# Kernel optimization log

Hardware: AMD Instinct MI355X
Metric: run time of the kernel (lower is better)

Reference implementation:

```python
import jax, jax.numpy as jnp
import numpy as np
import math

ROPE_THETA = 10000.0


def apply_rope(x, positions):
    # x: [B, H, S, d_k], positions: [S]
    d_k = x.shape[-1]
    inv_freq = 1.0 / (ROPE_THETA ** (jnp.arange(0, d_k, 2, dtype=jnp.float32) / d_k))  # [d_k/2]
    angles = positions.astype(jnp.float32)[:, None] * inv_freq[None, :]  # [S, d_k/2]
    cos = jnp.cos(angles)
    sin = jnp.sin(angles)
    x1 = x[..., 0::2]
    x2 = x[..., 1::2]
    r1 = x1 * cos - x2 * sin
    r2 = x1 * sin + x2 * cos
    out = jnp.stack([r1, r2], axis=-1)  # interleave pairs back
    return out.reshape(x.shape)


def setup_inputs() -> dict:
    key = jax.random.key(0)
    k1, k2, k3 = jax.random.split(key, 3)
    B, S, D = 4, 2048, 1024
    x = jax.random.normal(k1, (B, S, D), dtype=jnp.float32)
    token_positions = jnp.arange(S, dtype=jnp.int32)
    w_qkv = jax.random.normal(k2, (3 * D, D), dtype=jnp.float32) * (1.0 / math.sqrt(D))
    w_o = jax.random.normal(k3, (D, D), dtype=jnp.float32) * (1.0 / math.sqrt(D))
    return {"x": x, "token_positions": token_positions, "w_qkv": w_qkv, "w_o": w_o}


def reference(x, token_positions, w_qkv, w_o):
    B, S, D = x.shape
    H = 16
    d_k = D // H
    qkv = jnp.einsum('bsd,ed->bse', x, w_qkv)  # [B, S, 3D]
    # rearrange '... s (stack h dk) -> stack ... h s dk'
    qkv = qkv.reshape(B, S, 3, H, d_k)
    q = jnp.transpose(qkv[:, :, 0], (0, 2, 1, 3))  # [B, H, S, dk]
    k = jnp.transpose(qkv[:, :, 1], (0, 2, 1, 3))
    v = jnp.transpose(qkv[:, :, 2], (0, 2, 1, 3))
    q = apply_rope(q, token_positions)
    k = apply_rope(k, token_positions)
    scores = jnp.einsum('bhqd,bhkd->bhqk', q, k) / math.sqrt(d_k)
    causal = jnp.tril(jnp.ones((S, S), dtype=bool))
    scores = jnp.where(causal[None, None], scores, -jnp.inf)
    attn = jax.nn.softmax(scores, axis=-1)
    out = jnp.einsum('bhqk,bhkd->bhqd', attn, v)  # [B, H, S, dk]
    out = jnp.transpose(out, (0, 2, 1, 3)).reshape(B, S, D)
    return jnp.einsum('bsd,ed->bse', out, w_o)
```

## Files before the change

### kernel.cpp

```cpp
#include <hip/hip_runtime.h>
#include <hip/hip_bf16.h>
#include <math.h>

typedef __bf16 bf16_t;
typedef __attribute__((ext_vector_type(8))) __bf16 bf16x8;
typedef __attribute__((ext_vector_type(4))) __bf16 bf16x4;
typedef __attribute__((ext_vector_type(4))) float f32x4;

#define MFMA_16x16x32(A_, B_, C_) __builtin_amdgcn_mfma_f32_16x16x32_bf16((A_), (B_), (C_), 0, 0, 0)

#define Bsz 4
#define Ssz 2048
#define Dsz 1024
#define Hh 16
#define DKd 64
#define Mrows (Bsz * Ssz)
#define N1 (3 * Dsz)
#define KD Dsz

__global__ void cvt_f32_bf16_kernel(const float* __restrict__ src, bf16_t* __restrict__ dst, int n4) {
  int i = blockIdx.x * blockDim.x + threadIdx.x;
  if (i >= n4) return;
  float4 v = reinterpret_cast<const float4*>(src)[i];
  bf16x4 o = {(bf16_t)v.x, (bf16_t)v.y, (bf16_t)v.z, (bf16_t)v.w};
  reinterpret_cast<bf16x4*>(dst)[i] = o;
}

__global__ void rope_tab_kernel(const int* __restrict__ pos, float2* __restrict__ tab) {
  int i = blockIdx.x * blockDim.x + threadIdx.x;
  if (i >= Ssz * 32) return;
  int s = i >> 5, f = i & 31;
  float inv_freq = powf(10000.0f, -(float)(2 * f) / 64.0f);
  float a = (float)pos[s] * inv_freq;
  tab[i] = make_float2(cosf(a), sinf(a));
}

__global__ __launch_bounds__(512, 1) void gemm256_qkv_kernel(
    const bf16_t* __restrict__ A, const bf16_t* __restrict__ Bt,
    bf16_t* __restrict__ qb, bf16_t* __restrict__ kb, bf16_t* __restrict__ vtb,
    const float2* __restrict__ tab) {
  constexpr int NT = KD / 64;
  __shared__ __align__(16) bf16_t As[2][256 * 64];
  __shared__ __align__(16) bf16_t Bs[2][192 * 64];
  const int t = threadIdx.x;
  const int w = t >> 6, l = t & 63;
  const int lr = l & 15, lk = l >> 4;
  const int rs = lr >> 1;
  const int wm = w >> 2, wn = w & 3;
  const int m0 = blockIdx.y * 256, n0 = blockIdx.x * 192;

  const int gcol = ((t & 7) ^ ((t >> 4) & 7)) * 8;
  const bf16_t* gA = A + (size_t)(m0 + (t >> 3)) * KD + gcol;
  const bf16_t* gB = Bt + (size_t)(n0 + (t >> 3)) * KD + gcol;

  f32x4 acc[8][3] = {};
  bf16x8 bfv[3][2];

#define LDA_(I_, SB_, KT_)                                                        \
  __builtin_amdgcn_global_load_lds(gA + (size_t)(I_) * 64 * KD + (KT_),           \
                                   &As[SB_][((I_) * 64 + w * 8) * 64], 16, 0, 0)
#define LDB_(I_, SB_, KT_)                                                        \
  __builtin_amdgcn_global_load_lds(gB + (size_t)(I_) * 64 * KD + (KT_),           \
                                   &Bs[SB_][((I_) * 64 + w * 8) * 64], 16, 0, 0)

#define PH(BUF_, P_, STG0_, STG1_, VMW_)                                          \
  do {                                                                            \
    if ((P_) == 0) {                                                              \
      _Pragma("unroll") for (int n_ = 0; n_ < 3; ++n_) {                          \
        const int R_ = wn * 48 + n_ * 16 + lr;                                    \
        bfv[n_][0] = *reinterpret_cast<const bf16x8*>(                            \
            &Bs[BUF_][R_ * 64 + ((lk ^ rs) * 8)]);                                \
        bfv[n_][1] = *reinterpret_cast<const bf16x8*>(                            \
            &Bs[BUF_][R_ * 64 + (((4 + lk) ^ rs) * 8)]);                          \
      }                                                                           \
    }                                                                             \
    bf16x8 af0_[2], af1_[2];                                                      \
    {                                                                             \
      const int Ra_ = wm * 128 + (P_) * 32 + lr;                                  \
      const int Rb_ = Ra_ + 16;                                                   \
      af0_[0] = *reinterpret_cast<const bf16x8*>(&As[BUF_][Ra_ * 64 + ((lk ^ rs) * 8)]);       \
      af0_[1] = *reinterpret_cast<const bf16x8*>(&As[BUF_][Ra_ * 64 + (((4 + lk) ^ rs) * 8)]); \
      af1_[0] = *reinterpret_cast<const bf16x8*>(&As[BUF_][Rb_ * 64 + ((lk ^ rs) * 8)]);       \
      af1_[1] = *reinterpret_cast<const bf16x8*>(&As[BUF_][Rb_ * 64 + (((4 + lk) ^ rs) * 8)]); \
    }                                                                             \
    STG0_;                                                                        \
    STG1_;                                                                        \
    __builtin_amdgcn_s_barrier();                                                 \
    asm volatile("s_waitcnt lgkmcnt(0)" ::: "memory");                            \
    __builtin_amdgcn_sched_barrier(0);                                            \
    __builtin_amdgcn_s_setprio(1);                                                \
    _Pragma("unroll") for (int n_ = 0; n_ < 3; ++n_) {                            \
      acc[(P_)*2][n_] = MFMA_16x16x32(af0_[0], bfv[n_][0], acc[(P_)*2][n_]);      \
      acc[(P_)*2][n_] = MFMA_16x16x32(af0_[1], bfv[n_][1], acc[(P_)*2][n_]);      \
      acc[(P_)*2 + 1][n_] = MFMA_16x16x32(af1_[0], bfv[n_][0], acc[(P_)*2 + 1][n_]); \
      acc[(P_)*2 + 1][n_] = MFMA_16x16x32(af1_[1], bfv[n_][1], acc[(P_)*2 + 1][n_]); \
    }                                                                             \
    __builtin_amdgcn_s_setprio(0);                                                \
    VMW_;                                                                         \
    __builtin_amdgcn_s_barrier();                                                 \
  } while (0)

#define VM4_ do { asm volatile("s_waitcnt vmcnt(4)" ::: "memory"); __builtin_amdgcn_sched_barrier(0); } while (0)
#define VM2_ do { asm volatile("s_waitcnt vmcnt(2)" ::: "memory"); __builtin_amdgcn_sched_barrier(0); } while (0)

#define TILE_(BUF_, KTN_)                                                         \
  do {                                                                            \
    PH(BUF_, 0, LDB_(0, (BUF_) ^ 1, KTN_), LDB_(1, (BUF_) ^ 1, KTN_), (void)0);   \
    PH(BUF_, 1, LDB_(2, (BUF_) ^ 1, KTN_), LDA_(0, (BUF_) ^ 1, KTN_), VM4_);      \
    PH(BUF_, 2, LDA_(2, (BUF_) ^ 1, KTN_), LDA_(1, (BUF_) ^ 1, KTN_), (void)0);   \
    PH(BUF_, 3, LDA_(3, (BUF_) ^ 1, KTN_), (void)0, VM2_);                        \
  } while (0)

  LDB_(0, 0, 0); LDB_(1, 0, 0); LDB_(2, 0, 0);
  LDA_(0, 0, 0); LDA_(2, 0, 0); LDA_(1, 0, 0); LDA_(3, 0, 0);
  asm volatile("s_waitcnt vmcnt(2)" ::: "memory");
  __builtin_amdgcn_s_barrier();

#pragma unroll 1
  for (int tt = 0; tt < NT; tt += 2) {
    const int ktn0 = ((tt + 1) & (NT - 1)) * 64;
    TILE_(0, ktn0);
    const int ktn1 = ((tt + 2) & (NT - 1)) * 64;
    TILE_(1, ktn1);
  }
#undef TILE_
#undef VM4_
#undef VM2_
#undef PH
#undef LDA_
#undef LDB_

#pragma unroll
  for (int n = 0; n < 3; ++n) {
    const int colbase = n0 + wn * 48 + n * 16;
    const int sect = colbase >> 10;
    const int h = (colbase >> 6) & 15;
    const int dk = (colbase & 63) + lr;
    if (sect < 2) {
      bf16_t* dst0 = (sect == 0) ? qb : kb;
#pragma unroll
      for (int m = 0; m < 8; ++m)
#pragma unroll
        for (int r = 0; r < 4; ++r) {
          const int grow = m0 + wm * 128 + m * 16 + lk * 4 + r;
          const int bb = grow >> 11, s = grow & (Ssz - 1);
          const float v = acc[m][n][r];
          const float pv = __shfl_xor(v, 1);
          const float2 cs = tab[(s << 5) | (dk >> 1)];
          float vr = (dk & 1) ? (pv * cs.y + v * cs.x) : (v * cs.x - pv * cs.y);
          if (sect == 0) vr *= 0.125f;
          dst0[((size_t)(bb * Hh + h) * Ssz + s) * DKd + dk] = (bf16_t)vr;
        }
    } else {
#pragma unroll
      for (int m = 0; m < 8; ++m) {
        const int grow0 = m0 + wm * 128 + m * 16 + lk * 4;
        const int bb = grow0 >> 11, s0 = grow0 & (Ssz - 1);
        const bf16x4 ov = {(bf16_t)acc[m][n][0], (bf16_t)acc[m][n][1],
                           (bf16_t)acc[m][n][2], (bf16_t)acc[m][n][3]};
        *reinterpret_cast<bf16x4*>(
            vtb + ((size_t)(bb * Hh + h) * DKd + dk) * Ssz + s0) = ov;
      }
    }
  }
}

__global__ __launch_bounds__(512, 2) void gemm_out_kernel(
    const bf16_t* __restrict__ A, const bf16_t* __restrict__ Bt,
    float* __restrict__ fout) {
  constexpr int NT = KD / 64;
  __shared__ __align__(16) bf16_t As[2][256 * 64];
  __shared__ __align__(16) bf16_t Bs[2][128 * 64];
  const int t = threadIdx.x;
  const int w = t >> 6, l = t & 63;
  const int lr = l & 15, lk = l >> 4;
  const int rs = lr >> 1;
  const int wm = w >> 2, wn = w & 3;
  const int m0 = blockIdx.y * 256, n0 = blockIdx.x * 128;

  const int gcol = ((t & 7) ^ ((t >> 4) & 7)) * 8;
  const bf16_t* gA = A + (size_t)(m0 + (t >> 3)) * KD + gcol;
  const bf16_t* gB = Bt + (size_t)(n0 + (t >> 3)) * KD + gcol;

  f32x4 acc[8][2] = {};

#define OSTAGE(PH, KT)                                                                 \
  do {                                                                                 \
    _Pragma("unroll") for (int i = 0; i < 4; ++i)                                      \
        __builtin_amdgcn_global_load_lds(gA + (size_t)i * 64 * KD + (KT),              \
                                         &As[PH][(i * 64 + w * 8) * 64], 16, 0, 0);    \
    _Pragma("unroll") for (int i = 0; i < 2; ++i)                                      \
        __builtin_amdgcn_global_load_lds(gB + (size_t)i * 64 * KD + (KT),              \
                                         &Bs[PH][(i * 64 + w * 8) * 64], 16, 0, 0);    \
  } while (0)

  OSTAGE(0, 0);
  __syncthreads();
  for (int tt = 0; tt < NT; ++tt) {
    const int b = tt & 1;
    if (tt + 1 < NT) OSTAGE(b ^ 1, (tt + 1) * 64);
    bf16x8 bfv[2][2];
#pragma unroll
    for (int n = 0; n < 2; ++n) {
      const int R = wn * 32 + n * 16 + lr;
#pragma unroll
      for (int ks = 0; ks < 2; ++ks)
        bfv[n][ks] = *reinterpret_cast<const bf16x8*>(&Bs[b][R * 64 + (((ks * 4 + lk) ^ rs) * 8)]);
    }
#pragma unroll
    for (int mp = 0; mp < 4; ++mp) {
      bf16x8 af[2][2];
#pragma unroll
      for (int mi = 0; mi < 2; ++mi) {
        const int R = wm * 128 + (mp * 2 + mi) * 16 + lr;
#pragma unroll
        for (int ks = 0; ks < 2; ++ks)
          af[mi][ks] = *reinterpret_cast<const bf16x8*>(&As[b][R * 64 + (((ks * 4 + lk) ^ rs) * 8)]);
      }
      __builtin_amdgcn_s_setprio(1);
#pragma unroll
      for (int mi = 0; mi < 2; ++mi)
#pragma unroll
        for (int n = 0; n < 2; ++n) {
          acc[mp * 2 + mi][n] = MFMA_16x16x32(af[mi][0], bfv[n][0], acc[mp * 2 + mi][n]);
          acc[mp * 2 + mi][n] = MFMA_16x16x32(af[mi][1], bfv[n][1], acc[mp * 2 + mi][n]);
        }
      __builtin_amdgcn_s_setprio(0);
    }
    __syncthreads();
  }
#undef OSTAGE

#pragma unroll
  for (int m = 0; m < 8; ++m)
#pragma unroll
    for (int r = 0; r < 4; ++r) {
      const int grow = m0 + wm * 128 + m * 16 + lk * 4 + r;
      float* op = fout + (size_t)grow * Dsz + n0 + wn * 32 + lr;
      op[0] = acc[m][0][r];
      op[16] = acc[m][1][r];
    }
}

__global__ __launch_bounds__(256, 3) void attn_kernel(
    const bf16_t* __restrict__ qb, const bf16_t* __restrict__ kb,
    const bf16_t* __restrict__ vtb, bf16_t* __restrict__ aout) {
  __shared__ __align__(16) bf16_t Ks[64 * 64];
  __shared__ __align__(16) bf16_t Vs[64 * 64];
  const int t = threadIdx.x, w = t >> 6, l = t & 63;
  const int lr = l & 15, lk = l >> 4;
  const int bid = blockIdx.x;
  const int bh = (bid & 7) * 8 + ((bid >> 3) & 7);
  const int qt = 15 - (bid >> 6);
  const int q0 = qt * 128;
  const int sub0 = q0 + w * 32;

  const bf16_t* qbase = qb + ((size_t)bh * Ssz + sub0) * DKd;
  bf16x8 qf[2][2];
#pragma unroll
  for (int s = 0; s < 2; ++s) {
    qf[s][0] = *reinterpret_cast<const bf16x8*>(qbase + (s * 16 + lr) * DKd + lk * 8);
    qf[s][1] = *reinterpret_cast<const bf16x8*>(qbase + (s * 16 + lr) * DKd + 32 + lk * 8);
  }

  f32x4 o[2][4] = {};
  float mrow[2] = {-INFINITY, -INFINITY};
  float lsum[2] = {0.f, 0.f};

  const int srow = t >> 2;
  const int scc = (t & 3) * 2;
  const bf16_t* kg = kb + ((size_t)bh * Ssz + srow) * DKd + scc * 8;
  const bf16_t* vg = vtb + ((size_t)bh * DKd + srow) * Ssz + scc * 8;
  bf16_t* ksw0 = Ks + srow * 64 + ((scc ^ (srow & 7)) * 8);
  bf16_t* ksw1 = Ks + srow * 64 + (((scc + 1) ^ (srow & 7)) * 8);
  bf16_t* vw[4];
#pragma unroll
  for (int u = 0; u < 2; ++u) {
    const int c = scc + u;
    const int B = 32 * (c >> 2) + 16 * (c & 1) + 4 * ((c & 3) >> 1);
    const int ch = B >> 3, off = B & 7;
    vw[2 * u] = Vs + srow * 64 + ((ch ^ (srow & 7)) * 8) + off;
    vw[2 * u + 1] = Vs + srow * 64 + (((ch + 1) ^ (srow & 7)) * 8) + off;
  }

  const int kvend = q0 + 128;
  bf16x8 pk0 = *reinterpret_cast<const bf16x8*>(kg);
  bf16x8 pk1 = *reinterpret_cast<const bf16x8*>(kg + 8);
  bf16x8 pv0 = *reinterpret_cast<const bf16x8*>(vg);
  bf16x8 pv1 = *reinterpret_cast<const bf16x8*>(vg + 8);

  for (int kv = 0; kv < kvend; kv += 64) {
    __syncthreads();
    *reinterpret_cast<bf16x8*>(ksw0) = pk0;
    *reinterpret_cast<bf16x8*>(ksw1) = pk1;
    *reinterpret_cast<bf16x4*>(vw[0]) = __builtin_shufflevector(pv0, pv0, 0, 1, 2, 3);
    *reinterpret_cast<bf16x4*>(vw[1]) = __builtin_shufflevector(pv0, pv0, 4, 5, 6, 7);
    *reinterpret_cast<bf16x4*>(vw[2]) = __builtin_shufflevector(pv1, pv1, 0, 1, 2, 3);
    *reinterpret_cast<bf16x4*>(vw[3]) = __builtin_shufflevector(pv1, pv1, 4, 5, 6, 7);
    __syncthreads();
    if (kv + 64 < kvend) {
      pk0 = *reinterpret_cast<const bf16x8*>(kg + (size_t)(kv + 64) * DKd);
      pk1 = *reinterpret_cast<const bf16x8*>(kg + (size_t)(kv + 64) * DKd + 8);
      pv0 = *reinterpret_cast<const bf16x8*>(vg + kv + 64);
      pv1 = *reinterpret_cast<const bf16x8*>(vg + kv + 64 + 8);
    }
#pragma unroll
    for (int s = 0; s < 2; ++s) {
      const int subrow = sub0 + s * 16;
      if (kv > subrow + 15) continue;
      f32x4 sa[4];
#pragma unroll
      for (int n = 0; n < 4; ++n) {
        const int R = n * 16 + lr;
        const bf16x8 a0 = *reinterpret_cast<const bf16x8*>(Ks + R * 64 + ((lk ^ (R & 7)) * 8));
        const bf16x8 a1 = *reinterpret_cast<const bf16x8*>(Ks + R * 64 + (((lk + 4) ^ (R & 7)) * 8));
        f32x4 z = {};
        z = MFMA_16x16x32(a0, qf[s][0], z);
        z = MFMA_16x16x32(a1, qf[s][1], z);
        sa[n] = z;
      }
      if (kv + 63 > subrow) {
        const int qrow = subrow + lr;
        const int kbase = kv + lk * 4;
#pragma unroll
        for (int n = 0; n < 4; ++n)
#pragma unroll
          for (int r = 0; r < 4; ++r)
            if (kbase + n * 16 + r > qrow) sa[n][r] = -INFINITY;
      }
      float mx = fmaxf(fmaxf(fmaxf(sa[0][0], sa[0][1]), fmaxf(sa[0][2], sa[0][3])),
                       fmaxf(fmaxf(sa[1][0], sa[1][1]), fmaxf(sa[1][2], sa[1][3])));
      mx = fmaxf(mx, fmaxf(fmaxf(fmaxf(sa[2][0], sa[2][1]), fmaxf(sa[2][2], sa[2][3])),
                           fmaxf(fmaxf(sa[3][0], sa[3][1]), fmaxf(sa[3][2], sa[3][3]))));
      mx = fmaxf(mx, __shfl_xor(mx, 16));
      mx = fmaxf(mx, __shfl_xor(mx, 32));
      const float mnew = fmaxf(mrow[s], mx);
      const float scl = __expf(mrow[s] - mnew);
      mrow[s] = mnew;
      float ps = 0.f;
#pragma unroll
      for (int n = 0; n < 4; ++n)
#pragma unroll
        for (int r = 0; r < 4; ++r) {
          const float p = __expf(sa[n][r] - mnew);
          sa[n][r] = p;
          ps += p;
        }
      lsum[s] = lsum[s] * scl + ps;
#pragma unroll
      for (int n = 0; n < 4; ++n)
#pragma unroll
        for (int r = 0; r < 4; ++r) o[s][n][r] *= scl;
      bf16x8 pb0, pb1;
#pragma unroll
      for (int r = 0; r < 4; ++r) {
        pb0[r] = (bf16_t)sa[0][r];
        pb0[4 + r] = (bf16_t)sa[1][r];
        pb1[r] = (bf16_t)sa[2][r];
        pb1[4 + r] = (bf16_t)sa[3][r];
      }
#pragma unroll
      for (int n = 0; n < 4; ++n) {
        const int R = n * 16 + lr;
        const bf16x8 v0 = *reinterpret_cast<const bf16x8*>(Vs + R * 64 + ((lk ^ (R & 7)) * 8));
        const bf16x8 v1 = *reinterpret_cast<const bf16x8*>(Vs + R * 64 + (((lk + 4) ^ (R & 7)) * 8));
        o[s][n] = MFMA_16x16x32(v0, pb0, o[s][n]);
        o[s][n] = MFMA_16x16x32(v1, pb1, o[s][n]);
      }
    }
  }
  const int b_ = bh >> 4, h_ = bh & 15;
#pragma unroll
  for (int s = 0; s < 2; ++s) {
    float sm = lsum[s];
    sm += __shfl_xor(sm, 16);
    sm += __shfl_xor(sm, 32);
    const float inv = 1.0f / sm;
    const int qrow = sub0 + s * 16 + lr;
    bf16_t* op = aout + ((size_t)b_ * Ssz + qrow) * Dsz + h_ * DKd + lk * 4;
#pragma unroll
    for (int n = 0; n < 4; ++n) {
      const bf16x4 ov = {(bf16_t)(o[s][n][0] * inv), (bf16_t)(o[s][n][1] * inv),
                         (bf16_t)(o[s][n][2] * inv), (bf16_t)(o[s][n][3] * inv)};
      *reinterpret_cast<bf16x4*>(op + n * 16) = ov;
    }
  }
}

extern "C" void kernel_launch(void* const* d_in, const int* in_sizes, int n_in,
                              void* d_out, int out_size, void* d_ws, size_t ws_size,
                              hipStream_t stream) {
  const float* x = (const float*)d_in[0];
  const int* pos = (const int*)d_in[1];
  const float* wqkv = (const float*)d_in[2];
  const float* wo = (const float*)d_in[3];
  float* out = (float*)d_out;

  bf16_t* xb = (bf16_t*)d_ws;
  bf16_t* wqkvb = xb + (size_t)Mrows * KD;
  bf16_t* wob = wqkvb + (size_t)N1 * KD;
  bf16_t* qbuf = wob + (size_t)Dsz * KD;
  bf16_t* kbuf = qbuf + (size_t)64 * Ssz * DKd;
  bf16_t* vtb = kbuf + (size_t)64 * Ssz * DKd;
  float2* tab = (float2*)(vtb + (size_t)64 * Ssz * DKd);
  bf16_t* aout = xb;

  {
    int n4 = Mrows * KD / 4;
    cvt_f32_bf16_kernel<<<(n4 + 255) / 256, 256, 0, stream>>>(x, xb, n4);
  }
  {
    int n4 = N1 * KD / 4;
    cvt_f32_bf16_kernel<<<(n4 + 255) / 256, 256, 0, stream>>>(wqkv, wqkvb, n4);
  }
  {
    int n4 = Dsz * KD / 4;
    cvt_f32_bf16_kernel<<<(n4 + 255) / 256, 256, 0, stream>>>(wo, wob, n4);
  }
  rope_tab_kernel<<<(Ssz * 32 + 255) / 256, 256, 0, stream>>>(pos, tab);

  gemm256_qkv_kernel<<<dim3(N1 / 192, Mrows / 256), 512, 0, stream>>>(
      xb, wqkvb, qbuf, kbuf, vtb, tab);

  attn_kernel<<<dim3(16 * 64), 256, 0, stream>>>(qbuf, kbuf, vtb, aout);

  gemm_out_kernel<<<dim3(Dsz / 128, Mrows / 256), 512, 0, stream>>>(
      aout, wob, out);
}
```

Measured before the change: 179.0 us.

## Interleave staged loads with MFMA phases in out-proj GEMM; double-buffer attention K/V

The output-projection GEMM now splits each K-tile into four phases that issue parts of the next tile's global-to-LDS loads between MFMA groups, using explicit barriers, waitcnt and sched_barrier. Occupancy is set to one block per CU. The attention kernel double-buffers its K/V shared tiles, so each step needs one barrier instead of two and the LDS writes for the next tile happen after compute. The aim is to hide load latency and cut synchronisation stalls, at the cost of more LDS in attention and fragile manual waitcnt scheduling.

```diff
diff --git a/kernel.cpp b/kernel.cpp
--- a/kernel.cpp
+++ b/kernel.cpp
@@ -165,7 +165,7 @@
   }
 }
 
-__global__ __launch_bounds__(512, 2) void gemm_out_kernel(
+__global__ __launch_bounds__(512, 1) void gemm_out_kernel(
     const bf16_t* __restrict__ A, const bf16_t* __restrict__ Bt,
     float* __restrict__ fout) {
   constexpr int NT = KD / 64;
@@ -183,53 +183,81 @@
   const bf16_t* gB = Bt + (size_t)(n0 + (t >> 3)) * KD + gcol;
 
   f32x4 acc[8][2] = {};
-
-#define OSTAGE(PH, KT)                                                                 \
-  do {                                                                                 \
-    _Pragma("unroll") for (int i = 0; i < 4; ++i)                                      \
-        __builtin_amdgcn_global_load_lds(gA + (size_t)i * 64 * KD + (KT),              \
-                                         &As[PH][(i * 64 + w * 8) * 64], 16, 0, 0);    \
-    _Pragma("unroll") for (int i = 0; i < 2; ++i)                                      \
-        __builtin_amdgcn_global_load_lds(gB + (size_t)i * 64 * KD + (KT),              \
-                                         &Bs[PH][(i * 64 + w * 8) * 64], 16, 0, 0);    \
+  bf16x8 bfv[2][2];
+
+#define OLDA_(I_, SB_, KT_)                                                       \
+  __builtin_amdgcn_global_load_lds(gA + (size_t)(I_) * 64 * KD + (KT_),           \
+                                   &As[SB_][((I_) * 64 + w * 8) * 64], 16, 0, 0)
+#define OLDB_(I_, SB_, KT_)                                                       \
+  __builtin_amdgcn_global_load_lds(gB + (size_t)(I_) * 64 * KD + (KT_),           \
+                                   &Bs[SB_][((I_) * 64 + w * 8) * 64], 16, 0, 0)
+
+#define OPH(BUF_, P_, STG0_, STG1_, VMW_)                                         \
+  do {                                                                            \
+    if ((P_) == 0) {                                                              \
+      _Pragma("unroll") for (int n_ = 0; n_ < 2; ++n_) {                          \
+        const int R_ = wn * 32 + n_ * 16 + lr;                                    \
+        bfv[n_][0] = *reinterpret_cast<const bf16x8*>(                            \
+            &Bs[BUF_][R_ * 64 + ((lk ^ rs) * 8)]);                                \
+        bfv[n_][1] = *reinterpret_cast<const bf16x8*>(                            \
+            &Bs[BUF_][R_ * 64 + (((4 + lk) ^ rs) * 8)]);                          \
+      }                                                                           \
+    }                                                                             \
+    bf16x8 af0_[2], af1_[2];                                                      \
+    {                                                                             \
+      const int Ra_ = wm * 128 + (P_) * 32 + lr;                                  \
+      const int Rb_ = Ra_ + 16;                                                   \
+      af0_[0] = *reinterpret_cast<const bf16x8*>(&As[BUF_][Ra_ * 64 + ((lk ^ rs) * 8)]);       \
+      af0_[1] = *reinterpret_cast<const bf16x8*>(&As[BUF_][Ra_ * 64 + (((4 + lk) ^ rs) * 8)]); \
+      af1_[0] = *reinterpret_cast<const bf16x8*>(&As[BUF_][Rb_ * 64 + ((lk ^ rs) * 8)]);       \
+      af1_[1] = *reinterpret_cast<const bf16x8*>(&As[BUF_][Rb_ * 64 + (((4 + lk) ^ rs) * 8)]); \
+    }                                                                             \
+    STG0_;                                                                        \
+    STG1_;                                                                        \
+    __builtin_amdgcn_s_barrier();                                                 \
+    asm volatile("s_waitcnt lgkmcnt(0)" ::: "memory");                            \
+    __builtin_amdgcn_sched_barrier(0);                                            \
+    __builtin_amdgcn_s_setprio(1);                                                \
+    _Pragma("unroll") for (int n_ = 0; n_ < 2; ++n_) {                            \
+      acc[(P_)*2][n_] = MFMA_16x16x32(af0_[0], bfv[n_][0], acc[(P_)*2][n_]);      \
+      acc[(P_)*2][n_] = MFMA_16x16x32(af0_[1], bfv[n_][1], acc[(P_)*2][n_]);      \
+      acc[(P_)*2 + 1][n_] = MFMA_16x16x32(af1_[0], bfv[n_][0], acc[(P_)*2 + 1][n_]); \
+      acc[(P_)*2 + 1][n_] = MFMA_16x16x32(af1_[1], bfv[n_][1], acc[(P_)*2 + 1][n_]); \
+    }                                                                             \
+    __builtin_amdgcn_s_setprio(0);                                                \
+    VMW_;                                                                         \
+    __builtin_amdgcn_s_barrier();                                                 \
   } while (0)
 
-  OSTAGE(0, 0);
-  __syncthreads();
-  for (int tt = 0; tt < NT; ++tt) {
-    const int b = tt & 1;
-    if (tt + 1 < NT) OSTAGE(b ^ 1, (tt + 1) * 64);
-    bf16x8 bfv[2][2];
-#pragma unroll
-    for (int n = 0; n < 2; ++n) {
-      const int R = wn * 32 + n * 16 + lr;
-#pragma unroll
-      for (int ks = 0; ks < 2; ++ks)
-        bfv[n][ks] = *reinterpret_cast<const bf16x8*>(&Bs[b][R * 64 + (((ks * 4 + lk) ^ rs) * 8)]);
-    }
-#pragma unroll
-    for (int mp = 0; mp < 4; ++mp) {
-      bf16x8 af[2][2];
-#pragma unroll
-      for (int mi = 0; mi < 2; ++mi) {
-        const int R = wm * 128 + (mp * 2 + mi) * 16 + lr;
-#pragma unroll
-        for (int ks = 0; ks < 2; ++ks)
-          af[mi][ks] = *reinterpret_cast<const bf16x8*>(&As[b][R * 64 + (((ks * 4 + lk) ^ rs) * 8)]);
-      }
-      __builtin_amdgcn_s_setprio(1);
-#pragma unroll
-      for (int mi = 0; mi < 2; ++mi)
-#pragma unroll
-        for (int n = 0; n < 2; ++n) {
-          acc[mp * 2 + mi][n] = MFMA_16x16x32(af[mi][0], bfv[n][0], acc[mp * 2 + mi][n]);
-          acc[mp * 2 + mi][n] = MFMA_16x16x32(af[mi][1], bfv[n][1], acc[mp * 2 + mi][n]);
-        }
-      __builtin_amdgcn_s_setprio(0);
-    }
-    __syncthreads();
-  }
-#undef OSTAGE
+#define OVM4_ do { asm volatile("s_waitcnt vmcnt(4)" ::: "memory"); __builtin_amdgcn_sched_barrier(0); } while (0)
+#define OVM2_ do { asm volatile("s_waitcnt vmcnt(2)" ::: "memory"); __builtin_amdgcn_sched_barrier(0); } while (0)
+
+#define OTILE_(BUF_, KTN_)                                                        \
+  do {                                                                            \
+    OPH(BUF_, 0, OLDB_(0, (BUF_) ^ 1, KTN_), OLDB_(1, (BUF_) ^ 1, KTN_), (void)0);\
+    OPH(BUF_, 1, OLDA_(0, (BUF_) ^ 1, KTN_), OLDA_(2, (BUF_) ^ 1, KTN_), OVM4_);  \
+    OPH(BUF_, 2, OLDA_(1, (BUF_) ^ 1, KTN_), OLDA_(3, (BUF_) ^ 1, KTN_), (void)0);\
+    OPH(BUF_, 3, (void)0, (void)0, OVM2_);                                        \
+  } while (0)
+
+  OLDB_(0, 0, 0); OLDB_(1, 0, 0);
+  OLDA_(0, 0, 0); OLDA_(2, 0, 0); OLDA_(1, 0, 0); OLDA_(3, 0, 0);
+  asm volatile("s_waitcnt vmcnt(2)" ::: "memory");
+  __builtin_amdgcn_s_barrier();
+
+#pragma unroll 1
+  for (int tt = 0; tt < NT; tt += 2) {
+    const int ktn0 = ((tt + 1) & (NT - 1)) * 64;
+    OTILE_(0, ktn0);
+    const int ktn1 = ((tt + 2) & (NT - 1)) * 64;
+    OTILE_(1, ktn1);
+  }
+#undef OTILE_
+#undef OVM4_
+#undef OVM2_
+#undef OPH
+#undef OLDA_
+#undef OLDB_
 
 #pragma unroll
   for (int m = 0; m < 8; ++m)
@@ -245,8 +273,8 @@
 __global__ __launch_bounds__(256, 3) void attn_kernel(
     const bf16_t* __restrict__ qb, const bf16_t* __restrict__ kb,
     const bf16_t* __restrict__ vtb, bf16_t* __restrict__ aout) {
-  __shared__ __align__(16) bf16_t Ks[64 * 64];
-  __shared__ __align__(16) bf16_t Vs[64 * 64];
+  __shared__ __align__(16) bf16_t Ks[2][64 * 64];
+  __shared__ __align__(16) bf16_t Vs[2][64 * 64];
   const int t = threadIdx.x, w = t >> 6, l = t & 63;
   const int lr = l & 15, lk = l >> 4;
   const int bid = blockIdx.x;
@@ -271,16 +299,16 @@
   const int scc = (t & 3) * 2;
   const bf16_t* kg = kb + ((size_t)bh * Ssz + srow) * DKd + scc * 8;
   const bf16_t* vg = vtb + ((size_t)bh * DKd + srow) * Ssz + scc * 8;
-  bf16_t* ksw0 = Ks + srow * 64 + ((scc ^ (srow & 7)) * 8);
-  bf16_t* ksw1 = Ks + srow * 64 + (((scc + 1) ^ (srow & 7)) * 8);
-  bf16_t* vw[4];
+  const int koff0 = srow * 64 + ((scc ^ (srow & 7)) * 8);
+  const int koff1 = srow * 64 + (((scc + 1) ^ (srow & 7)) * 8);
+  int voff[4];
 #pragma unroll
   for (int u = 0; u < 2; ++u) {
     const int c = scc + u;
     const int B = 32 * (c >> 2) + 16 * (c & 1) + 4 * ((c & 3) >> 1);
     const int ch = B >> 3, off = B & 7;
-    vw[2 * u] = Vs + srow * 64 + ((ch ^ (srow & 7)) * 8) + off;
-    vw[2 * u + 1] = Vs + srow * 64 + (((ch + 1) ^ (srow & 7)) * 8) + off;
+    voff[2 * u] = srow * 64 + ((ch ^ (srow & 7)) * 8) + off;
+    voff[2 * u + 1] = srow * 64 + (((ch + 1) ^ (srow & 7)) * 8) + off;
   }
 
   const int kvend = q0 + 128;
@@ -289,21 +317,25 @@
   bf16x8 pv0 = *reinterpret_cast<const bf16x8*>(vg);
   bf16x8 pv1 = *reinterpret_cast<const bf16x8*>(vg + 8);
 
+  *reinterpret_cast<bf16x8*>(&Ks[0][koff0]) = pk0;
+  *reinterpret_cast<bf16x8*>(&Ks[0][koff1]) = pk1;
+  *reinterpret_cast<bf16x4*>(&Vs[0][voff[0]]) = __builtin_shufflevector(pv0, pv0, 0, 1, 2, 3);
+  *reinterpret_cast<bf16x4*>(&Vs[0][voff[1]]) = __builtin_shufflevector(pv0, pv0, 4, 5, 6, 7);
+  *reinterpret_cast<bf16x4*>(&Vs[0][voff[2]]) = __builtin_shufflevector(pv1, pv1, 0, 1, 2, 3);
+  *reinterpret_cast<bf16x4*>(&Vs[0][voff[3]]) = __builtin_shufflevector(pv1, pv1, 4, 5, 6, 7);
+  __syncthreads();
+
   for (int kv = 0; kv < kvend; kv += 64) {
-    __syncthreads();
-    *reinterpret_cast<bf16x8*>(ksw0) = pk0;
-    *reinterpret_cast<bf16x8*>(ksw1) = pk1;
-    *reinterpret_cast<bf16x4*>(vw[0]) = __builtin_shufflevector(pv0, pv0, 0, 1, 2, 3);
-    *reinterpret_cast<bf16x4*>(vw[1]) = __builtin_shufflevector(pv0, pv0, 4, 5, 6, 7);
-    *reinterpret_cast<bf16x4*>(vw[2]) = __builtin_shufflevector(pv1, pv1, 0, 1, 2, 3);
-    *reinterpret_cast<bf16x4*>(vw[3]) = __builtin_shufflevector(pv1, pv1, 4, 5, 6, 7);
-    __syncthreads();
-    if (kv + 64 < kvend) {
+    const int buf = (kv >> 6) & 1;
+    const bool more = (kv + 64 < kvend);
+    if (more) {
       pk0 = *reinterpret_cast<const bf16x8*>(kg + (size_t)(kv + 64) * DKd);
       pk1 = *reinterpret_cast<const bf16x8*>(kg + (size_t)(kv + 64) * DKd + 8);
       pv0 = *reinterpret_cast<const bf16x8*>(vg + kv + 64);
       pv1 = *reinterpret_cast<const bf16x8*>(vg + kv + 64 + 8);
     }
+    const bf16_t* Kb = Ks[buf];
+    const bf16_t* Vb = Vs[buf];
 #pragma unroll
     for (int s = 0; s < 2; ++s) {
       const int subrow = sub0 + s * 16;
@@ -312,8 +344,8 @@
 #pragma unroll
       for (int n = 0; n < 4; ++n) {
         const int R = n * 16 + lr;
-        const bf16x8 a0 = *reinterpret_cast<const bf16x8*>(Ks + R * 64 + ((lk ^ (R & 7)) * 8));
-        const bf16x8 a1 = *reinterpret_cast<const bf16x8*>(Ks + R * 64 + (((lk + 4) ^ (R & 7)) * 8));
+        const bf16x8 a0 = *reinterpret_cast<const bf16x8*>(Kb + R * 64 + ((lk ^ (R & 7)) * 8));
+        const bf16x8 a1 = *reinterpret_cast<const bf16x8*>(Kb + R * 64 + (((lk + 4) ^ (R & 7)) * 8));
         f32x4 z = {};
         z = MFMA_16x16x32(a0, qf[s][0], z);
         z = MFMA_16x16x32(a1, qf[s][1], z);
@@ -362,11 +394,22 @@
 #pragma unroll
       for (int n = 0; n < 4; ++n) {
         const int R = n * 16 + lr;
-        const bf16x8 v0 = *reinterpret_cast<const bf16x8*>(Vs + R * 64 + ((lk ^ (R & 7)) * 8));
-        const bf16x8 v1 = *reinterpret_cast<const bf16x8*>(Vs + R * 64 + (((lk + 4) ^ (R & 7)) * 8));
+        const bf16x8 v0 = *reinterpret_cast<const bf16x8*>(Vb + R * 64 + ((lk ^ (R & 7)) * 8));
+        const bf16x8 v1 = *reinterpret_cast<const bf16x8*>(Vb + R * 64 + (((lk + 4) ^ (R & 7)) * 8));
         o[s][n] = MFMA_16x16x32(v0, pb0, o[s][n]);
         o[s][n] = MFMA_16x16x32(v1, pb1, o[s][n]);
       }
+    }
+    if (more) {
+      bf16_t* Kn = Ks[buf ^ 1];
+      bf16_t* Vn = Vs[buf ^ 1];
+      *reinterpret_cast<bf16x8*>(&Kn[koff0]) = pk0;
+      *reinterpret_cast<bf16x8*>(&Kn[koff1]) = pk1;
+      *reinterpret_cast<bf16x4*>(&Vn[voff[0]]) = __builtin_shufflevector(pv0, pv0, 0, 1, 2, 3);
+      *reinterpret_cast<bf16x4*>(&Vn[voff[1]]) = __builtin_shufflevector(pv0, pv0, 4, 5, 6, 7);
+      *reinterpret_cast<bf16x4*>(&Vn[voff[2]]) = __builtin_shufflevector(pv1, pv1, 0, 1, 2, 3);
+      *reinterpret_cast<bf16x4*>(&Vn[voff[3]]) = __builtin_shufflevector(pv1, pv1, 4, 5, 6, 7);
+      __syncthreads();
     }
   }
   const int b_ = bh >> 4, h_ = bh & 15;
```

New measurement: 178.5 us. About the same (-0.3%).
